# Performance work log

Hardware: AMD Instinct MI355X
Metric: run time of the kernel (lower is better)

Reference implementation:

```python
import jax, jax.numpy as jnp
import numpy as np

N_NODES = 100000
N_EDGES = 640000
D = 128
EPS = 1e-5

def _full_layer_norm(x):
    # torch layer_norm with normalized_shape == x.shape: stats over ALL elements
    mu = jnp.mean(x)
    var = jnp.mean(jnp.square(x - mu))  # biased variance
    return (x - mu) * jax.lax.rsqrt(var + EPS)

def setup_inputs() -> dict:
    key = jax.random.key(0)
    k1, k2, k3, k4, k5 = jax.random.split(key, 5)
    scale1 = 1.0 / np.sqrt(D)
    scale2 = 1.0 / np.sqrt(2 * D)
    return {
        "edge_features": jax.random.normal(k1, (N_EDGES, D), dtype=jnp.float32),
        "node_features": jax.random.normal(k2, (N_NODES, D), dtype=jnp.float32),
        "edge_indices": jax.random.randint(k3, (N_EDGES, 2), 0, N_NODES, dtype=jnp.int32),
        "W1": jax.random.normal(k4, (D, D), dtype=jnp.float32) * scale1,
        "b1": jnp.zeros((D,), dtype=jnp.float32),
        "W2": jax.random.normal(k5, (2 * D, D), dtype=jnp.float32) * scale2,
        "b2": jnp.zeros((D,), dtype=jnp.float32),
    }

def reference(edge_features, node_features, edge_indices, W1, b1, W2, b2):
    # node MLP: linear -> whole-tensor layernorm -> gelu
    h = node_features @ W1 + b1                       # [N, D]
    h = jax.nn.gelu(_full_layer_norm(h), approximate=False)
    # gather source-node features onto edges
    src = edge_indices[:, 0]
    dst = edge_indices[:, 1]
    gathered = h[src]                                 # [E, D]
    e = jnp.concatenate([edge_features, gathered], axis=1)  # [E, 2D]
    e = e @ W2 + b2                                   # [E, D]
    e = jax.nn.gelu(_full_layer_norm(e), approximate=False)
    # scatter-mean (include_self=False): nodes with no in-edges stay 0
    seg_sum = jax.ops.segment_sum(e, dst, num_segments=N_NODES)       # [N, D]
    counts = jax.ops.segment_sum(jnp.ones((e.shape[0],), e.dtype), dst,
                                 num_segments=N_NODES)                 # [N]
    counts = counts[:, None]
    return jnp.where(counts > 0, seg_sum / jnp.maximum(counts, 1.0), 0.0)
```

## Files before the change

### kernel.cpp

```cpp
#include <hip/hip_runtime.h>
#include <hip/hip_bf16.h>
#include <math.h>

typedef __bf16 bf16;
typedef bf16 bf16x8 __attribute__((ext_vector_type(8)));
typedef float f32x4 __attribute__((ext_vector_type(4)));
typedef unsigned short ushort_t;
typedef unsigned long long u64;

#define N_NODES 100000
#define N_EDGES 640000
#define DD 128
#define MAXDEG 64
#define STAT_SCALE 1048576.0

__device__ __forceinline__ float gelu_fast(float x) {
    float z2 = x * (1.595769122f + 0.071354816f * x * x);
    return x * __builtin_amdgcn_rcpf(1.0f + __expf(-z2));
}

__device__ __forceinline__ ushort_t bf16_bits(float x) {
    bf16 h = (bf16)x;
    return __builtin_bit_cast(ushort_t, h);
}

__device__ __forceinline__ float bits_to_f(ushort_t u) {
    return __uint_as_float(((unsigned)u) << 16);
}

__device__ __forceinline__ long long to_fixed(double x) {
    return (long long)(x * STAT_SCALE + (x >= 0.0 ? 0.5 : -0.5));
}

__device__ __forceinline__ void stats_atomic(float lsum, float lsq, float* red,
                                             u64* dsum, u64* dsq) {
    int tid = threadIdx.x;
    red[tid] = lsum; __syncthreads();
    for (int s = 128; s > 0; s >>= 1) { if (tid < s) red[tid] += red[tid + s]; __syncthreads(); }
    float bs = red[0]; __syncthreads();
    red[tid] = lsq; __syncthreads();
    for (int s = 128; s > 0; s >>= 1) { if (tid < s) red[tid] += red[tid + s]; __syncthreads(); }
    if (tid == 0) {
        atomicAdd(dsum, (u64)to_fixed((double)bs));
        atomicAdd(dsq,  (u64)to_fixed((double)red[0]));
    }
}

__device__ __forceinline__ void stats_decode(const u64* stats, double cnt,
                                             float* mu, float* rs) {
    long long ss = (long long)stats[0], sq = (long long)stats[1];
    double mu_d = ((double)ss / STAT_SCALE) / cnt;
    double var  = ((double)sq / STAT_SCALE) / cnt - mu_d * mu_d;
    *mu = (float)mu_d;
    *rs = (float)(1.0 / sqrt(var + 1e-5));
}

#define PACK8(dstp, a, b) { \
    ushort_t o_[8] = {bf16_bits(a.x), bf16_bits(a.y), bf16_bits(a.z), bf16_bits(a.w), \
                      bf16_bits(b.x), bf16_bits(b.y), bf16_bits(b.z), bf16_bits(b.w)}; \
    *(uint4*)(dstp) = *(const uint4*)o_; }

__global__ __launch_bounds__(256) void k0_init(int* __restrict__ cnt,
                                               u64* __restrict__ stats)
{
    int i = blockIdx.x * 256 + threadIdx.x;
    if (i < N_NODES) cnt[i] = 0;
    if (i < 4) stats[i] = 0ull;
}

#define K1_TILES 1563
__global__ __launch_bounds__(256) void k1_gemm1(
    const float* __restrict__ nf, const float* __restrict__ W1,
    const float* __restrict__ b1, ushort_t* __restrict__ hpre,
    u64* __restrict__ stats, int nblocks)
{
    __shared__ bf16 Ash[64 * 136];
    __shared__ float red[256];
    const int tid = threadIdx.x;
    const int lane = tid & 63;
    const int w = tid >> 6;
    const int l15 = lane & 15, l4 = lane >> 4;

    bf16x8 bfrag[4][2];
    #pragma unroll
    for (int s = 0; s < 4; ++s)
        #pragma unroll
        for (int t = 0; t < 2; ++t) {
            int n = w * 32 + t * 16 + l15;
            #pragma unroll
            for (int j = 0; j < 8; ++j)
                bfrag[s][t][j] = (bf16)W1[(s * 32 + l4 * 8 + j) * DD + n];
        }
    float4 bias4[2];
    bias4[0] = *(const float4*)&b1[w * 32 + l4 * 4];
    bias4[1] = *(const float4*)&b1[w * 32 + 16 + l4 * 4];

    float lsum = 0.f, lsq = 0.f;
    const int srow = tid >> 2;
    const int q = tid & 3;

    float4 efr[8];
    {
        int grow = min(blockIdx.x * 64 + srow, N_NODES - 1);
        const float4* p = (const float4*)&nf[(size_t)grow * DD + q * 32];
        #pragma unroll
        for (int u = 0; u < 8; ++u) efr[u] = p[u];
    }

    for (int tile = blockIdx.x; tile < K1_TILES; tile += nblocks) {
        const int rbase = tile * 64;
        __syncthreads();
        #pragma unroll
        for (int u = 0; u < 4; ++u)
            PACK8(&Ash[srow * 136 + q * 32 + u * 8], efr[2 * u], efr[2 * u + 1]);
        __syncthreads();
        int nt = tile + nblocks;
        if (nt < K1_TILES) {
            int grow = min(nt * 64 + srow, N_NODES - 1);
            const float4* p = (const float4*)&nf[(size_t)grow * DD + q * 32];
            #pragma unroll
            for (int u = 0; u < 8; ++u) efr[u] = p[u];
        }
        f32x4 acc[4][2];
        #pragma unroll
        for (int r = 0; r < 4; ++r)
            #pragma unroll
            for (int t = 0; t < 2; ++t)
                acc[r][t] = (f32x4){0.f, 0.f, 0.f, 0.f};
        #pragma unroll
        for (int s = 0; s < 4; ++s)
            #pragma unroll
            for (int r = 0; r < 4; ++r) {
                bf16x8 a = *(const bf16x8*)&Ash[(r * 16 + l15) * 136 + s * 32 + l4 * 8];
                acc[r][0] = __builtin_amdgcn_mfma_f32_16x16x32_bf16(bfrag[s][0], a, acc[r][0], 0, 0, 0);
                acc[r][1] = __builtin_amdgcn_mfma_f32_16x16x32_bf16(bfrag[s][1], a, acc[r][1], 0, 0, 0);
            }
        #pragma unroll
        for (int r = 0; r < 4; ++r) {
            int row = rbase + r * 16 + l15;
            if (row < N_NODES) {
                #pragma unroll
                for (int t = 0; t < 2; ++t) {
                    int col = w * 32 + t * 16 + l4 * 4;
                    ushort_t o[4];
                    #pragma unroll
                    for (int j = 0; j < 4; ++j) {
                        float v = acc[r][t][j] + bias4[t][j];
                        lsum += v; lsq += v * v;
                        o[j] = bf16_bits(v);
                    }
                    *(uint2*)&hpre[(size_t)row * DD + col] = *(const uint2*)o;
                }
            }
        }
    }
    stats_atomic(lsum, lsq, red, &stats[0], &stats[1]);
}

__global__ __launch_bounds__(256) void k2b_gemmh(
    const ushort_t* __restrict__ hpre, const float* __restrict__ W2,
    const u64* __restrict__ stats, ushort_t* __restrict__ hh, int nblocks)
{
    __shared__ bf16 Ash[64 * 136];
    float mu, rs;
    stats_decode(stats, (double)N_NODES * DD, &mu, &rs);

    const int tid = threadIdx.x;
    const int lane = tid & 63;
    const int w = tid >> 6;
    const int l15 = lane & 15, l4 = lane >> 4;

    bf16x8 bfrag[4][2];
    #pragma unroll
    for (int s = 0; s < 4; ++s)
        #pragma unroll
        for (int t = 0; t < 2; ++t) {
            int n = w * 32 + t * 16 + l15;
            #pragma unroll
            for (int j = 0; j < 8; ++j)
                bfrag[s][t][j] = (bf16)W2[(DD + s * 32 + l4 * 8 + j) * DD + n];
        }

    const int srow = tid >> 2;
    const int q = tid & 3;

    uint4 hr[4];
    {
        int grow = min(blockIdx.x * 64 + srow, N_NODES - 1);
        const uint4* p = (const uint4*)&hpre[(size_t)grow * DD + q * 32];
        #pragma unroll
        for (int u = 0; u < 4; ++u) hr[u] = p[u];
    }

    for (int tile = blockIdx.x; tile < K1_TILES; tile += nblocks) {
        const int rbase = tile * 64;
        __syncthreads();
        #pragma unroll
        for (int u = 0; u < 4; ++u) {
            const ushort_t* in = (const ushort_t*)&hr[u];
            ushort_t o[8];
            #pragma unroll
            for (int j = 0; j < 8; ++j)
                o[j] = bf16_bits(gelu_fast((bits_to_f(in[j]) - mu) * rs));
            *(uint4*)&Ash[srow * 136 + q * 32 + u * 8] = *(const uint4*)o;
        }
        __syncthreads();
        int nt = tile + nblocks;
        if (nt < K1_TILES) {
            int grow = min(nt * 64 + srow, N_NODES - 1);
            const uint4* p = (const uint4*)&hpre[(size_t)grow * DD + q * 32];
            #pragma unroll
            for (int u = 0; u < 4; ++u) hr[u] = p[u];
        }
        f32x4 acc[4][2];
        #pragma unroll
        for (int r = 0; r < 4; ++r)
            #pragma unroll
            for (int t = 0; t < 2; ++t)
                acc[r][t] = (f32x4){0.f, 0.f, 0.f, 0.f};
        #pragma unroll
        for (int s = 0; s < 4; ++s)
            #pragma unroll
            for (int r = 0; r < 4; ++r) {
                bf16x8 a = *(const bf16x8*)&Ash[(r * 16 + l15) * 136 + s * 32 + l4 * 8];
                acc[r][0] = __builtin_amdgcn_mfma_f32_16x16x32_bf16(bfrag[s][0], a, acc[r][0], 0, 0, 0);
                acc[r][1] = __builtin_amdgcn_mfma_f32_16x16x32_bf16(bfrag[s][1], a, acc[r][1], 0, 0, 0);
            }
        #pragma unroll
        for (int r = 0; r < 4; ++r) {
            int row = rbase + r * 16 + l15;
            if (row < N_NODES) {
                #pragma unroll
                for (int t = 0; t < 2; ++t) {
                    int col = w * 32 + t * 16 + l4 * 4;
                    ushort_t o[4];
                    #pragma unroll
                    for (int j = 0; j < 4; ++j)
                        o[j] = bf16_bits(acc[r][t][j]);
                    *(uint2*)&hh[(size_t)row * DD + col] = *(const uint2*)o;
                }
            }
        }
    }
}

#define K4_TILES (N_EDGES / 64)
__global__ __launch_bounds__(256) void k4_gemm2(
    const float* __restrict__ ef, const ushort_t* __restrict__ hh,
    const int* __restrict__ eidx, const float* __restrict__ W2,
    const float* __restrict__ b2, ushort_t* __restrict__ e0,
    u64* __restrict__ stats, int nblocks)
{
    __shared__ bf16 Ash[64 * 136];
    __shared__ float red[256];
    const int tid = threadIdx.x;
    const int lane = tid & 63;
    const int w = tid >> 6;
    const int l15 = lane & 15, l4 = lane >> 4;

    bf16x8 bfrag[4][2];
    #pragma unroll
    for (int s = 0; s < 4; ++s)
        #pragma unroll
        for (int t = 0; t < 2; ++t) {
            int n = w * 32 + t * 16 + l15;
            #pragma unroll
            for (int j = 0; j < 8; ++j)
                bfrag[s][t][j] = (bf16)W2[(s * 32 + l4 * 8 + j) * DD + n];
        }
    float4 bias4[2];
    bias4[0] = *(const float4*)&b2[w * 32 + l4 * 4];
    bias4[1] = *(const float4*)&b2[w * 32 + 16 + l4 * 4];

    float lsum = 0.f, lsq = 0.f;
    const int srow = tid >> 2;
    const int q = tid & 3;

    float4 efr[8];
    {
        const float4* p = (const float4*)&ef[(size_t)(blockIdx.x * 64 + srow) * DD + q * 32];
        #pragma unroll
        for (int u = 0; u < 8; ++u) efr[u] = p[u];
    }

    for (int tile = blockIdx.x; tile < K4_TILES; tile += nblocks) {
        const int ebase = tile * 64;
        int srcv[4];
        #pragma unroll
        for (int r = 0; r < 4; ++r)
            srcv[r] = eidx[(size_t)(ebase + r * 16 + l15) * 2];
        uint2 hv[4][2];
        #pragma unroll
        for (int r = 0; r < 4; ++r)
            #pragma unroll
            for (int t = 0; t < 2; ++t)
                hv[r][t] = *(const uint2*)&hh[(size_t)srcv[r] * DD + w * 32 + t * 16 + l4 * 4];
        __syncthreads();
        #pragma unroll
        for (int u = 0; u < 4; ++u)
            PACK8(&Ash[srow * 136 + q * 32 + u * 8], efr[2 * u], efr[2 * u + 1]);
        __syncthreads();
        int nt = tile + nblocks;
        if (nt < K4_TILES) {
            const float4* p = (const float4*)&ef[(size_t)(nt * 64 + srow) * DD + q * 32];
            #pragma unroll
            for (int u = 0; u < 8; ++u) efr[u] = p[u];
        }
        f32x4 acc[4][2];
        #pragma unroll
        for (int r = 0; r < 4; ++r)
            #pragma unroll
            for (int t = 0; t < 2; ++t)
                acc[r][t] = (f32x4){0.f, 0.f, 0.f, 0.f};
        #pragma unroll
        for (int s = 0; s < 4; ++s)
            #pragma unroll
            for (int r = 0; r < 4; ++r) {
                bf16x8 a = *(const bf16x8*)&Ash[(r * 16 + l15) * 136 + s * 32 + l4 * 8];
                acc[r][0] = __builtin_amdgcn_mfma_f32_16x16x32_bf16(bfrag[s][0], a, acc[r][0], 0, 0, 0);
                acc[r][1] = __builtin_amdgcn_mfma_f32_16x16x32_bf16(bfrag[s][1], a, acc[r][1], 0, 0, 0);
            }
        #pragma unroll
        for (int r = 0; r < 4; ++r) {
            int row = ebase + r * 16 + l15;
            #pragma unroll
            for (int t = 0; t < 2; ++t) {
                int col = w * 32 + t * 16 + l4 * 4;
                float hadd[4] = {bits_to_f((ushort_t)(hv[r][t].x & 0xffff)),
                                 bits_to_f((ushort_t)(hv[r][t].x >> 16)),
                                 bits_to_f((ushort_t)(hv[r][t].y & 0xffff)),
                                 bits_to_f((ushort_t)(hv[r][t].y >> 16))};
                ushort_t o[4];
                #pragma unroll
                for (int j = 0; j < 4; ++j) {
                    float v = acc[r][t][j] + bias4[t][j] + hadd[j];
                    lsum += v; lsq += v * v;
                    o[j] = bf16_bits(v);
                }
                *(uint2*)&e0[(size_t)row * DD + col] = *(const uint2*)o;
            }
        }
    }
    stats_atomic(lsum, lsq, red, &stats[2], &stats[3]);
}

__global__ __launch_bounds__(256) void k7_fill(
    const int* __restrict__ eidx, int* __restrict__ cnt, int* __restrict__ slot)
{
    int e = blockIdx.x * 256 + threadIdx.x;
    if (e >= N_EDGES) return;
    int dst = eidx[(size_t)e * 2 + 1];
    int pos = atomicAdd(&cnt[dst], 1);
    if (pos < MAXDEG) slot[dst * MAXDEG + pos] = e;
}

__global__ __launch_bounds__(256) void k8_gather(
    const ushort_t* __restrict__ e0v, const int* __restrict__ slot,
    const int* __restrict__ cnt, const u64* __restrict__ stats,
    float* __restrict__ out)
{
    float mu, rs;
    stats_decode(stats + 2, (double)N_EDGES * DD, &mu, &rs);
    int node = (int)((blockIdx.x * 256 + threadIdx.x) >> 6);
    int lane = threadIdx.x & 63;
    if (node >= N_NODES) return;
    const int hl = lane >> 5;
    const int l31 = lane & 31;
    int c = cnt[node];
    int m = min(c, MAXDEG);
    int myslot = (lane < m) ? slot[node * MAXDEG + lane] : 0;
    float a0 = 0.f, a1 = 0.f, a2 = 0.f, a3 = 0.f;
    const size_t off = (size_t)(l31 * 4);

    int steps = m >> 1;
    int s = 0;
    for (; s + 2 <= steps; s += 2) {
        int eA = __shfl(myslot, 2 * s + hl);
        int eB = __shfl(myslot, 2 * (s + 1) + hl);
        uint2 uA = *(const uint2*)&e0v[(size_t)eA * DD + off];
        uint2 uB = *(const uint2*)&e0v[(size_t)eB * DD + off];
        a0 += gelu_fast((__uint_as_float(uA.x << 16) - mu) * rs);
        a1 += gelu_fast((__uint_as_float(uA.x & 0xffff0000u) - mu) * rs);
        a2 += gelu_fast((__uint_as_float(uA.y << 16) - mu) * rs);
        a3 += gelu_fast((__uint_as_float(uA.y & 0xffff0000u) - mu) * rs);
        a0 += gelu_fast((__uint_as_float(uB.x << 16) - mu) * rs);
        a1 += gelu_fast((__uint_as_float(uB.x & 0xffff0000u) - mu) * rs);
        a2 += gelu_fast((__uint_as_float(uB.y << 16) - mu) * rs);
        a3 += gelu_fast((__uint_as_float(uB.y & 0xffff0000u) - mu) * rs);
    }
    for (; s < steps; ++s) {
        int eA = __shfl(myslot, 2 * s + hl);
        uint2 uA = *(const uint2*)&e0v[(size_t)eA * DD + off];
        a0 += gelu_fast((__uint_as_float(uA.x << 16) - mu) * rs);
        a1 += gelu_fast((__uint_as_float(uA.x & 0xffff0000u) - mu) * rs);
        a2 += gelu_fast((__uint_as_float(uA.y << 16) - mu) * rs);
        a3 += gelu_fast((__uint_as_float(uA.y & 0xffff0000u) - mu) * rs);
    }
    if (m & 1) {
        int eA = __shfl(myslot, m - 1);
        uint2 uA = *(const uint2*)&e0v[(size_t)eA * DD + off];
        float g0 = gelu_fast((__uint_as_float(uA.x << 16) - mu) * rs);
        float g1 = gelu_fast((__uint_as_float(uA.x & 0xffff0000u) - mu) * rs);
        float g2 = gelu_fast((__uint_as_float(uA.y << 16) - mu) * rs);
        float g3 = gelu_fast((__uint_as_float(uA.y & 0xffff0000u) - mu) * rs);
        if (hl == 0) { a0 += g0; a1 += g1; a2 += g2; a3 += g3; }
    }
    a0 += __shfl_xor(a0, 32);
    a1 += __shfl_xor(a1, 32);
    a2 += __shfl_xor(a2, 32);
    a3 += __shfl_xor(a3, 32);
    if (hl == 0) {
        float inv = c > 0 ? 1.0f / (float)c : 0.f;
        float4 res = {a0 * inv, a1 * inv, a2 * inv, a3 * inv};
        *(float4*)&out[(size_t)node * DD + l31 * 4] = res;
    }
}

extern "C" void kernel_launch(void* const* d_in, const int* in_sizes, int n_in,
                              void* d_out, int out_size, void* d_ws, size_t ws_size,
                              hipStream_t stream) {
    const float* ef  = (const float*)d_in[0];
    const float* nf  = (const float*)d_in[1];
    const int*   eix = (const int*)d_in[2];
    const float* W1  = (const float*)d_in[3];
    const float* b1  = (const float*)d_in[4];
    const float* W2  = (const float*)d_in[5];
    const float* b2  = (const float*)d_in[6];
    float* out = (float*)d_out;
    char* ws = (char*)d_ws;

    ushort_t* hpre  = (ushort_t*)(ws + 0);
    ushort_t* hh    = (ushort_t*)(ws + 25600000);
    ushort_t* e0    = (ushort_t*)(ws + 51200000);
    int*      cnt   = (int*)(ws + 215040000);
    u64*      stats = (u64*)(ws + 215440000);
    int*      slot  = (int*)(ws + 215440064);

    k0_init<<<391, 256, 0, stream>>>(cnt, stats);
    k1_gemm1<<<782, 256, 0, stream>>>(nf, W1, b1, hpre, stats, 782);
    k2b_gemmh<<<782, 256, 0, stream>>>(hpre, W2, stats, hh, 782);
    k7_fill<<<2500, 256, 0, stream>>>(eix, cnt, slot);
    k4_gemm2<<<2500, 256, 0, stream>>>(ef, hh, eix, W2, b2, e0, stats, 2500);
    k8_gather<<<25000, 256, 0, stream>>>(e0, slot, cnt, stats, out);
}
```

Baseline: 306.7 us.

## Restructure edge GEMM to per-wave 16-row tiles with W2 staged in LDS

The edge GEMM kernel now gives each wave its own 16-edge tile. Edge features are loaded straight from global memory into MFMA A-fragments, with no LDS staging or block-wide barriers per tile. The B operand (first half of W2) is converted to bf16 once per block and held in LDS, and all 128 output columns are computed per wave. The bias b2 is folded into the node-side projection kernel, and the fill kernel is launched earlier. The per-tile syncthreads and LDS A writes go away, in exchange for more LDS B reads per MFMA and less cross-wave register reuse of edge-feature loads.

```diff
diff --git a/kernel.cpp b/kernel.cpp
--- a/kernel.cpp
+++ b/kernel.cpp
@@ -159,7 +159,8 @@
 
 __global__ __launch_bounds__(256) void k2b_gemmh(
     const ushort_t* __restrict__ hpre, const float* __restrict__ W2,
-    const u64* __restrict__ stats, ushort_t* __restrict__ hh, int nblocks)
+    const float* __restrict__ b2, const u64* __restrict__ stats,
+    ushort_t* __restrict__ hh, int nblocks)
 {
     __shared__ bf16 Ash[64 * 136];
     float mu, rs;
@@ -180,6 +181,9 @@
             for (int j = 0; j < 8; ++j)
                 bfrag[s][t][j] = (bf16)W2[(DD + s * 32 + l4 * 8 + j) * DD + n];
         }
+    float4 bias4[2];
+    bias4[0] = *(const float4*)&b2[w * 32 + l4 * 4];
+    bias4[1] = *(const float4*)&b2[w * 32 + 16 + l4 * 4];
 
     const int srow = tid >> 2;
     const int q = tid & 3;
@@ -236,7 +240,7 @@
                     ushort_t o[4];
                     #pragma unroll
                     for (int j = 0; j < 4; ++j)
-                        o[j] = bf16_bits(acc[r][t][j]);
+                        o[j] = bf16_bits(acc[r][t][j] + bias4[t][j]);
                     *(uint2*)&hh[(size_t)row * DD + col] = *(const uint2*)o;
                 }
             }
@@ -244,101 +248,81 @@
     }
 }
 
-#define K4_TILES (N_EDGES / 64)
+#define K4_WTILES (N_EDGES / 16)
 __global__ __launch_bounds__(256) void k4_gemm2(
     const float* __restrict__ ef, const ushort_t* __restrict__ hh,
     const int* __restrict__ eidx, const float* __restrict__ W2,
-    const float* __restrict__ b2, ushort_t* __restrict__ e0,
-    u64* __restrict__ stats, int nblocks)
-{
-    __shared__ bf16 Ash[64 * 136];
+    ushort_t* __restrict__ e0, u64* __restrict__ stats, int nblocks)
+{
+    __shared__ bf16 Bsh[128 * 136];
     __shared__ float red[256];
     const int tid = threadIdx.x;
     const int lane = tid & 63;
     const int w = tid >> 6;
     const int l15 = lane & 15, l4 = lane >> 4;
 
-    bf16x8 bfrag[4][2];
-    #pragma unroll
-    for (int s = 0; s < 4; ++s)
-        #pragma unroll
-        for (int t = 0; t < 2; ++t) {
-            int n = w * 32 + t * 16 + l15;
+    if (tid < 128) {
+        int n = tid;
+        #pragma unroll
+        for (int kb = 0; kb < 16; ++kb) {
+            float v[8];
             #pragma unroll
             for (int j = 0; j < 8; ++j)
-                bfrag[s][t][j] = (bf16)W2[(s * 32 + l4 * 8 + j) * DD + n];
-        }
-    float4 bias4[2];
-    bias4[0] = *(const float4*)&b2[w * 32 + l4 * 4];
-    bias4[1] = *(const float4*)&b2[w * 32 + 16 + l4 * 4];
+                v[j] = W2[(size_t)(kb * 8 + j) * DD + n];
+            ushort_t o[8];
+            #pragma unroll
+            for (int j = 0; j < 8; ++j) o[j] = bf16_bits(v[j]);
+            *(uint4*)&Bsh[n * 136 + kb * 8] = *(const uint4*)o;
+        }
+    }
+    __syncthreads();
 
     float lsum = 0.f, lsq = 0.f;
-    const int srow = tid >> 2;
-    const int q = tid & 3;
-
-    float4 efr[8];
-    {
-        const float4* p = (const float4*)&ef[(size_t)(blockIdx.x * 64 + srow) * DD + q * 32];
-        #pragma unroll
-        for (int u = 0; u < 8; ++u) efr[u] = p[u];
-    }
-
-    for (int tile = blockIdx.x; tile < K4_TILES; tile += nblocks) {
-        const int ebase = tile * 64;
-        int srcv[4];
-        #pragma unroll
-        for (int r = 0; r < 4; ++r)
-            srcv[r] = eidx[(size_t)(ebase + r * 16 + l15) * 2];
-        uint2 hv[4][2];
-        #pragma unroll
-        for (int r = 0; r < 4; ++r)
-            #pragma unroll
-            for (int t = 0; t < 2; ++t)
-                hv[r][t] = *(const uint2*)&hh[(size_t)srcv[r] * DD + w * 32 + t * 16 + l4 * 4];
-        __syncthreads();
-        #pragma unroll
-        for (int u = 0; u < 4; ++u)
-            PACK8(&Ash[srow * 136 + q * 32 + u * 8], efr[2 * u], efr[2 * u + 1]);
-        __syncthreads();
-        int nt = tile + nblocks;
-        if (nt < K4_TILES) {
-            const float4* p = (const float4*)&ef[(size_t)(nt * 64 + srow) * DD + q * 32];
-            #pragma unroll
-            for (int u = 0; u < 8; ++u) efr[u] = p[u];
-        }
-        f32x4 acc[4][2];
-        #pragma unroll
-        for (int r = 0; r < 4; ++r)
-            #pragma unroll
-            for (int t = 0; t < 2; ++t)
-                acc[r][t] = (f32x4){0.f, 0.f, 0.f, 0.f};
-        #pragma unroll
-        for (int s = 0; s < 4; ++s)
-            #pragma unroll
-            for (int r = 0; r < 4; ++r) {
-                bf16x8 a = *(const bf16x8*)&Ash[(r * 16 + l15) * 136 + s * 32 + l4 * 8];
-                acc[r][0] = __builtin_amdgcn_mfma_f32_16x16x32_bf16(bfrag[s][0], a, acc[r][0], 0, 0, 0);
-                acc[r][1] = __builtin_amdgcn_mfma_f32_16x16x32_bf16(bfrag[s][1], a, acc[r][1], 0, 0, 0);
-            }
-        #pragma unroll
-        for (int r = 0; r < 4; ++r) {
-            int row = ebase + r * 16 + l15;
-            #pragma unroll
-            for (int t = 0; t < 2; ++t) {
-                int col = w * 32 + t * 16 + l4 * 4;
-                float hadd[4] = {bits_to_f((ushort_t)(hv[r][t].x & 0xffff)),
-                                 bits_to_f((ushort_t)(hv[r][t].x >> 16)),
-                                 bits_to_f((ushort_t)(hv[r][t].y & 0xffff)),
-                                 bits_to_f((ushort_t)(hv[r][t].y >> 16))};
-                ushort_t o[4];
-                #pragma unroll
-                for (int j = 0; j < 4; ++j) {
-                    float v = acc[r][t][j] + bias4[t][j] + hadd[j];
-                    lsum += v; lsq += v * v;
-                    o[j] = bf16_bits(v);
-                }
-                *(uint2*)&e0[(size_t)row * DD + col] = *(const uint2*)o;
-            }
+
+    for (int g = blockIdx.x * 4 + w; g < K4_WTILES; g += nblocks * 4) {
+        const int row = g * 16 + l15;
+        int src = eidx[(size_t)row * 2];
+        float4 a0[4], a1[4];
+        #pragma unroll
+        for (int s = 0; s < 4; ++s) {
+            const float4* pa = (const float4*)&ef[(size_t)row * DD + s * 32 + l4 * 8];
+            a0[s] = pa[0]; a1[s] = pa[1];
+        }
+        uint2 hv[8];
+        #pragma unroll
+        for (int t = 0; t < 8; ++t)
+            hv[t] = *(const uint2*)&hh[(size_t)src * DD + t * 16 + l4 * 4];
+
+        f32x4 acc[8];
+        #pragma unroll
+        for (int t = 0; t < 8; ++t) acc[t] = (f32x4){0.f, 0.f, 0.f, 0.f};
+
+        #pragma unroll
+        for (int s = 0; s < 4; ++s) {
+            ushort_t af[8] = {bf16_bits(a0[s].x), bf16_bits(a0[s].y), bf16_bits(a0[s].z), bf16_bits(a0[s].w),
+                              bf16_bits(a1[s].x), bf16_bits(a1[s].y), bf16_bits(a1[s].z), bf16_bits(a1[s].w)};
+            bf16x8 afrag = *(const bf16x8*)af;
+            #pragma unroll
+            for (int t = 0; t < 8; ++t) {
+                bf16x8 bfrag = *(const bf16x8*)&Bsh[(t * 16 + l15) * 136 + s * 32 + l4 * 8];
+                acc[t] = __builtin_amdgcn_mfma_f32_16x16x32_bf16(bfrag, afrag, acc[t], 0, 0, 0);
+            }
+        }
+
+        #pragma unroll
+        for (int t = 0; t < 8; ++t) {
+            float hadd[4] = {bits_to_f((ushort_t)(hv[t].x & 0xffff)),
+                             bits_to_f((ushort_t)(hv[t].x >> 16)),
+                             bits_to_f((ushort_t)(hv[t].y & 0xffff)),
+                             bits_to_f((ushort_t)(hv[t].y >> 16))};
+            ushort_t o[4];
+            #pragma unroll
+            for (int j = 0; j < 4; ++j) {
+                float v = acc[t][j] + hadd[j];
+                lsum += v; lsq += v * v;
+                o[j] = bf16_bits(v);
+            }
+            *(uint2*)&e0[(size_t)row * DD + t * 16 + l4 * 4] = *(const uint2*)o;
         }
     }
     stats_atomic(lsum, lsq, red, &stats[2], &stats[3]);
@@ -437,9 +421,9 @@
     int*      slot  = (int*)(ws + 215440064);
 
     k0_init<<<391, 256, 0, stream>>>(cnt, stats);
+    k7_fill<<<2500, 256, 0, stream>>>(eix, cnt, slot);
     k1_gemm1<<<782, 256, 0, stream>>>(nf, W1, b1, hpre, stats, 782);
-    k2b_gemmh<<<782, 256, 0, stream>>>(hpre, W2, stats, hh, 782);
-    k7_fill<<<2500, 256, 0, stream>>>(eix, cnt, slot);
-    k4_gemm2<<<2500, 256, 0, stream>>>(ef, hh, eix, W2, b2, e0, stats, 2500);
+    k2b_gemmh<<<782, 256, 0, stream>>>(hpre, W2, b2, stats, hh, 782);
+    k4_gemm2<<<2500, 256, 0, stream>>>(ef, hh, eix, W2, e0, stats, 2500);
     k8_gather<<<25000, 256, 0, stream>>>(e0, slot, cnt, stats, out);
 }
```

After: 322.5 us. +5.1%, slower.
